# Kernel tuning notes

Measured on AMD Instinct MI355X. Metric: run time of the kernel, lower is better.

## Reference

```python
import jax, jax.numpy as jnp
import numpy as np

H = 256
W = 256
CHUNK = 100  # faces per rasterizer scan step


def _cross2(o, p, q):
    # 2D cross product of (p-o) x (q-o); broadcasts over leading dims
    return (p[..., 0] - o[..., 0]) * (q[..., 1] - o[..., 1]) - (p[..., 1] - o[..., 1]) * (q[..., 0] - o[..., 0])


def transform(verts, K, Rt):
    # verts [B,V,3] -> pixel coords [B,V,3] = (x_pix, y_pix, z_cam)
    v_cam = jnp.einsum('bij,bnj->bni', Rt[:, :, :3], verts) + Rt[:, None, :, 3]
    v_proj = jnp.einsum('bij,bnj->bni', K, v_cam)
    z = v_cam[..., 2:3]
    return jnp.concatenate([v_proj[..., :2] / z, z], axis=-1)


def _pixel_centers(h, w, dtype):
    px = jnp.arange(w, dtype=dtype) + 0.5
    py = jnp.arange(h, dtype=dtype) + 0.5
    gx, gy = jnp.meshgrid(px, py, indexing='xy')  # [h,w]
    return gx, gy


def rasterize(v_pix, vi, h, w):
    # z-buffered triangle rasterization -> index image [B,h,w] (int32, -1 = bg)
    B = v_pix.shape[0]
    Fc = vi.shape[0]
    gx, gy = _pixel_centers(h, w, v_pix.dtype)
    pix = jnp.stack([gx.ravel(), gy.ravel()], axis=-1)  # [HW,2]
    face_ids = jnp.arange(Fc, dtype=jnp.int32).reshape(-1, CHUNK)
    inf = jnp.asarray(jnp.inf, v_pix.dtype)

    def step(carry, fids):
        best_z, best_i = carry
        tri = vi[fids]                      # [C,3]
        p = v_pix[:, tri]                   # [B,C,3,3]
        a, b, c = p[:, :, 0], p[:, :, 1], p[:, :, 2]
        area = _cross2(a[..., :2], b[..., :2], c[..., :2])  # [B,C]
        pixb = pix[None, None]              # [1,1,HW,2]
        w0 = _cross2(b[..., None, :2], c[..., None, :2], pixb)  # [B,C,HW]
        w1 = _cross2(c[..., None, :2], a[..., None, :2], pixb)
        w2 = _cross2(a[..., None, :2], b[..., None, :2], pixb)
        s = jnp.sign(area)[..., None]
        nz = jnp.abs(area)[..., None] > 1e-8
        inside = (w0 * s >= 0) & (w1 * s >= 0) & (w2 * s >= 0) & nz
        za, zb, zc = a[..., 2:3], b[..., 2:3], c[..., 2:3]
        valid = inside & (za > 0) & (zb > 0) & (zc > 0)
        ar = jnp.where(jnp.abs(area) > 1e-8, area, 1.0)[..., None]
        invz = (w0 / ar) / za + (w1 / ar) / zb + (w2 / ar) / zc  # persp-correct 1/z
        z = jnp.where(valid & (invz > 0), 1.0 / jnp.maximum(invz, 1e-12), inf)
        cz = z.min(axis=1)                  # [B,HW]
        ci = z.argmin(axis=1)
        cf = fids[ci]
        upd = cz < best_z
        return (jnp.where(upd, cz, best_z), jnp.where(upd, cf, best_i)), None

    init = (jnp.full((B, h * w), jnp.inf, v_pix.dtype), jnp.full((B, h * w), -1, jnp.int32))
    (_, bi), _ = jax.lax.scan(step, init, face_ids)
    return bi.reshape(B, h, w)


def render(v_pix, vi, index_img):
    # depth [B,h,w] and perspective-correct barycentrics [B,3,h,w]
    B, h, w = index_img.shape
    tri = vi[jnp.clip(index_img, 0)]                 # [B,h,w,3]
    p = jax.vmap(lambda v, t: v[t])(v_pix, tri)      # [B,h,w,3,3]
    gx, gy = _pixel_centers(h, w, v_pix.dtype)
    pt = jnp.stack([gx, gy], axis=-1)[None]          # [1,h,w,2]
    a, b, c = p[..., 0, :], p[..., 1, :], p[..., 2, :]
    w0 = _cross2(b[..., :2], c[..., :2], pt)
    w1 = _cross2(c[..., :2], a[..., :2], pt)
    w2 = _cross2(a[..., :2], b[..., :2], pt)
    area = w0 + w1 + w2
    ar = jnp.where(jnp.abs(area) > 1e-8, area, 1.0)
    f0 = (w0 / ar) / jnp.maximum(a[..., 2], 1e-8)
    f1 = (w1 / ar) / jnp.maximum(b[..., 2], 1e-8)
    f2 = (w2 / ar) / jnp.maximum(c[..., 2], 1e-8)
    invz = f0 + f1 + f2
    invz_s = jnp.where(jnp.abs(invz) > 1e-12, invz, 1.0)
    depth = 1.0 / invz_s
    bary = jnp.stack([f0, f1, f2], axis=-1) / invz_s[..., None]  # [B,h,w,3]
    m = index_img != -1
    depth_img = jnp.where(m, depth, 0.0)
    bary_img = jnp.where(m[..., None], bary, 0.0).transpose(0, 3, 1, 2)  # [B,3,h,w]
    return depth_img, bary_img


def interpolate(attr, vti, index_img, bary_img):
    # attr [B,N,D], bary_img [B,3,h,w] -> [B,D,h,w]
    tri = vti[jnp.clip(index_img, 0)]                # [B,h,w,3]
    av = jax.vmap(lambda a, t: a[t])(attr, tri)      # [B,h,w,3,D]
    return jnp.einsum('bhwkd,bkhw->bdhw', av, bary_img)


def grid_sample_bilinear(tex, grid):
    # tex [B,C,Ht,Wt], grid [B,h,w,2] in [-1,1]; align_corners=False, zero pad
    B, C, Ht, Wt = tex.shape
    x = (grid[..., 0] + 1.0) * Wt / 2.0 - 0.5
    y = (grid[..., 1] + 1.0) * Ht / 2.0 - 0.5
    x0 = jnp.floor(x)
    y0 = jnp.floor(y)
    wx = (x - x0)[:, None]
    wy = (y - y0)[:, None]
    x0i = x0.astype(jnp.int32)
    y0i = y0.astype(jnp.int32)

    def gat(ix, iy):
        valid = (ix >= 0) & (ix < Wt) & (iy >= 0) & (iy < Ht)
        ixc = jnp.clip(ix, 0, Wt - 1)
        iyc = jnp.clip(iy, 0, Ht - 1)
        v = jax.vmap(lambda t, yy, xx: t[:, yy, xx])(tex, iyc, ixc)  # [B,C,h,w]
        return v * valid[:, None].astype(tex.dtype)

    return (gat(x0i, y0i) * (1 - wx) * (1 - wy)
            + gat(x0i + 1, y0i) * wx * (1 - wy)
            + gat(x0i, y0i + 1) * (1 - wx) * wy
            + gat(x0i + 1, y0i + 1) * wx * wy)


def reference(verts, tex, K, Rt, vt, vi, vti):
    v_pix = transform(verts, K, Rt)
    index_img = jax.lax.stop_gradient(rasterize(v_pix, vi, H, W))
    depth_img, bary_img = render(v_pix, vi, index_img)
    B = verts.shape[0]
    vt_attr = jnp.broadcast_to((vt * 2.0 - 1.0)[None], (B,) + vt.shape)
    vt_img = interpolate(vt_attr, vti, index_img, bary_img)    # [B,2,H,W]
    mask = (index_img != -1)[:, None].astype(tex.dtype)
    img = grid_sample_bilinear(tex, vt_img.transpose(0, 2, 3, 1)) * mask
    # edge_grad_estimator is identity in the forward pass
    return img, depth_img, v_pix, vt_img, index_img, bary_img, mask


def setup_inputs() -> dict:
    key = jax.random.key(0)
    ks = jax.random.split(key, 6)
    B, V, Fc, Nvt = 2, 5000, 10000, 5000
    xy = jax.random.uniform(ks[0], (B, V, 2), minval=-1.5, maxval=1.5)
    z = jax.random.uniform(ks[1], (B, V, 1), minval=2.0, maxval=4.0)
    verts = jnp.concatenate([xy, z], axis=-1)
    tex = jax.random.uniform(ks[2], (B, 3, 1024, 1024), dtype=jnp.float32)
    K = jnp.broadcast_to(jnp.array([[256., 0., 128.], [0., 256., 128.], [0., 0., 1.]], dtype=jnp.float32), (B, 3, 3))
    Rt = jnp.broadcast_to(jnp.concatenate([jnp.eye(3, dtype=jnp.float32), jnp.zeros((3, 1), jnp.float32)], axis=1), (B, 3, 4))
    vt = jax.random.uniform(ks[3], (Nvt, 2), dtype=jnp.float32)
    vi = jax.random.randint(ks[4], (Fc, 3), 0, V).astype(jnp.int32)
    vti = jax.random.randint(ks[5], (Fc, 3), 0, Nvt).astype(jnp.int32)
    return {"verts": verts, "tex": tex, "K": K, "Rt": Rt, "vt": vt, "vi": vi, "vti": vti}
```

## Files before the change

kernel.cpp:

```cpp
#include <hip/hip_runtime.h>
#include <cmath>

#define H_ 256
#define W_ 256
#define SEG 4
#define NB 256
#define ILV 8
#define REC_STRIDE 24
#define INITKEY 0x7f800000FFFFFFFFull

__device__ inline unsigned fkey(float f) {
  unsigned u = __float_as_uint(f);
  return (u & 0x80000000u) ? ~u : (u | 0x80000000u);
}
__device__ inline float unfkey(unsigned k) {
  return (k & 0x80000000u) ? __uint_as_float(k & 0x7fffffffu) : __uint_as_float(~k);
}

__global__ void k_transform(const float* __restrict__ verts, const float* __restrict__ Km,
                            const float* __restrict__ Rt, float* __restrict__ vpix,
                            int B, int V) {
  int i = blockIdx.x * blockDim.x + threadIdx.x;
  if (i >= B * V) return;
  int b = i / V;
  float x = verts[(size_t)i * 3 + 0], y = verts[(size_t)i * 3 + 1], z = verts[(size_t)i * 3 + 2];
  const float* R = Rt + (size_t)b * 12;
  float cx = __fadd_rn(__fadd_rn(__fadd_rn(__fmul_rn(R[0], x), __fmul_rn(R[1], y)), __fmul_rn(R[2], z)), R[3]);
  float cy = __fadd_rn(__fadd_rn(__fadd_rn(__fmul_rn(R[4], x), __fmul_rn(R[5], y)), __fmul_rn(R[6], z)), R[7]);
  float cz = __fadd_rn(__fadd_rn(__fadd_rn(__fmul_rn(R[8], x), __fmul_rn(R[9], y)), __fmul_rn(R[10], z)), R[11]);
  const float* Kb = Km + (size_t)b * 9;
  float px = __fadd_rn(__fadd_rn(__fmul_rn(Kb[0], cx), __fmul_rn(Kb[1], cy)), __fmul_rn(Kb[2], cz));
  float py = __fadd_rn(__fadd_rn(__fmul_rn(Kb[3], cx), __fmul_rn(Kb[4], cy)), __fmul_rn(Kb[5], cz));
  vpix[(size_t)i * 3 + 0] = __fdiv_rn(px, cz);
  vpix[(size_t)i * 3 + 1] = __fdiv_rn(py, cz);
  vpix[(size_t)i * 3 + 2] = cz;
}

__global__ void k_init(unsigned long long* __restrict__ keys, int nkeys,
                       int* __restrict__ hist, int* __restrict__ cursor, int nbkt,
                       unsigned* __restrict__ minmax) {
  int i = blockIdx.x * blockDim.x + threadIdx.x;
  if (keys && i < nkeys) keys[i] = INITKEY;
  if (i < nbkt) { hist[i] = 0; cursor[i] = 0; }
  if (i == 0 && minmax) { minmax[0] = 0xFFFFFFFFu; minmax[1] = 0u; }
}

__global__ void k_faceprep(const float* __restrict__ vpix, const int* __restrict__ vi,
                           float* __restrict__ rec, unsigned* __restrict__ minmax,
                           int B, int V, int F) {
  int i = blockIdx.x * blockDim.x + threadIdx.x;
  if (i >= B * F) return;
  int b = i / F, f = i - b * F;
  int i0 = vi[f * 3 + 0], i1 = vi[f * 3 + 1], i2 = vi[f * 3 + 2];
  const float* base = vpix + (size_t)b * V * 3;
  float ax = base[(size_t)i0 * 3], ay = base[(size_t)i0 * 3 + 1], az = base[(size_t)i0 * 3 + 2];
  float bx = base[(size_t)i1 * 3], by = base[(size_t)i1 * 3 + 1], bz = base[(size_t)i1 * 3 + 2];
  float cx = base[(size_t)i2 * 3], cy = base[(size_t)i2 * 3 + 1], cz = base[(size_t)i2 * 3 + 2];
  float e0x = __fsub_rn(cx, bx), e0y = __fsub_rn(cy, by);
  float e1x = __fsub_rn(ax, cx), e1y = __fsub_rn(ay, cy);
  float e2x = __fsub_rn(bx, ax), e2y = __fsub_rn(by, ay);
  float area = __fsub_rn(__fmul_rn(e2x, __fsub_rn(cy, ay)), __fmul_rn(e2y, __fsub_rn(cx, ax)));
  float s = (area > 0.f) ? 1.f : ((area < 0.f) ? -1.f : 0.f);
  bool nz = fabsf(area) > 1e-8f;
  bool zv = (az > 0.f) && (bz > 0.f) && (cz > 0.f);
  float sprime = (nz && zv) ? s : __uint_as_float(0x7fc00000u);
  float ar = nz ? area : 1.0f;
  float zmin = fminf(az, fminf(bz, cz));
  float* r = rec + (size_t)i * REC_STRIDE;
  r[0] = ax; r[1] = ay; r[2] = bx; r[3] = by; r[4] = cx; r[5] = cy;
  r[6] = e0x; r[7] = e0y; r[8] = e1x; r[9] = e1y; r[10] = e2x; r[11] = e2y;
  r[12] = az; r[13] = bz; r[14] = cz; r[15] = sprime; r[16] = ar;
  r[17] = fminf(ax, fminf(bx, cx));
  r[18] = fmaxf(ax, fmaxf(bx, cx));
  r[19] = fminf(ay, fminf(by, cy));
  r[20] = fmaxf(ay, fmaxf(by, cy));
  r[21] = zmin; r[22] = 0.f; r[23] = 0.f;
  if (minmax && zmin == zmin) {
    unsigned k = fkey(zmin);
    atomicMin(&minmax[0], k);
    atomicMax(&minmax[1], k);
  }
}

__global__ void k_hist(const float* __restrict__ rec, const unsigned* __restrict__ minmax,
                       int* __restrict__ hist, int B, int F) {
  int i = blockIdx.x * blockDim.x + threadIdx.x;
  if (i >= B * F) return;
  int b = i / F;
  float zmin = rec[(size_t)i * REC_STRIDE + 21];
  float zlo = unfkey(minmax[0]), zhi = unfkey(minmax[1]);
  float scale = (float)NB / fmaxf(zhi - zlo, 1e-12f);
  int bkt = 0;
  if (zmin == zmin) bkt = min(NB - 1, max(0, (int)((zmin - zlo) * scale)));
  atomicAdd(&hist[b * NB + bkt], 1);
}

__global__ void k_scan(const int* __restrict__ hist, int* __restrict__ boff, int B) {
  __shared__ int sh[NB];
  int t = threadIdx.x;
  for (int b = 0; b < B; ++b) {
    sh[t] = hist[b * NB + t];
    __syncthreads();
    int self = sh[t];
    for (int ofs = 1; ofs < NB; ofs <<= 1) {
      int u = (t >= ofs) ? sh[t - ofs] : 0;
      __syncthreads();
      sh[t] += u;
      __syncthreads();
    }
    boff[b * NB + t] = sh[t] - self;
    __syncthreads();
  }
}

__global__ void k_scatter(const float* __restrict__ rec, const unsigned* __restrict__ minmax,
                          const int* __restrict__ boff, int* __restrict__ cursor,
                          float4* __restrict__ sA, float4* __restrict__ sB4,
                          float4* __restrict__ sC, float4* __restrict__ sZ,
                          float4* __restrict__ sbb, int* __restrict__ sfid,
                          int B, int F) {
  int i = blockIdx.x * blockDim.x + threadIdx.x;
  if (i >= B * F) return;
  int b = i / F, f = i - b * F;
  const float* r = rec + (size_t)i * REC_STRIDE;
  float zmin = r[21];
  float zlo = unfkey(minmax[0]), zhi = unfkey(minmax[1]);
  float rng = fmaxf(zhi - zlo, 1e-12f);
  float scale = (float)NB / rng;
  int bkt = 0;
  if (zmin == zmin) bkt = min(NB - 1, max(0, (int)((zmin - zlo) * scale)));
  int pos = boff[b * NB + bkt] + atomicAdd(&cursor[b * NB + bkt], 1);
  size_t gp = (size_t)b * F + pos;
  float sp = r[15];
  sbb[gp] = make_float4(r[17], r[18], r[19], r[20]);
  sA[gp]  = make_float4(r[0], r[1], r[2], r[3]);
  sB4[gp] = make_float4(r[4], r[5], __fmul_rn(sp, r[6]), __fmul_rn(sp, r[7]));
  sC[gp]  = make_float4(__fmul_rn(sp, r[8]), __fmul_rn(sp, r[9]),
                        __fmul_rn(sp, r[10]), __fmul_rn(sp, r[11]));
  sZ[gp]  = make_float4(r[12], r[13], r[14], __fmul_rn(sp, r[16]));
  sfid[gp] = f;
}

__global__ __launch_bounds__(64 * ILV) void k_raster_tile(const float4* __restrict__ sA,
                                                          const float4* __restrict__ sB4,
                                                          const float4* __restrict__ sC,
                                                          const float4* __restrict__ sZ,
                                                          const float4* __restrict__ sbb,
                                                          const int* __restrict__ sfid,
                                                          const int* __restrict__ boff,
                                                          const unsigned* __restrict__ minmax,
                                                          float* __restrict__ o_idx,
                                                          int B, int F) {
  int seg = blockIdx.x;
  int y   = blockIdx.y;
  int b   = blockIdx.z;
  int tid = threadIdx.x;
  int w = tid >> 6, lane = tid & 63;
  __shared__ unsigned long long sk[64];
  __shared__ int bstart[NB + 1];
  if (tid < 64) sk[tid] = INITKEY;
  if (tid < NB) bstart[tid] = boff[b * NB + tid];
  if (tid == 0) bstart[NB] = F;
  __syncthreads();
  float zlo = unfkey(minmax[0]), zhi = unfkey(minmax[1]);
  float rng = fmaxf(zhi - zlo, 1e-12f);
  float stepv = __fdiv_rn(rng, (float)NB);
  size_t fb = (size_t)b * F;
  float px = seg * 64 + lane + 0.5f, py = y + 0.5f;
  float wx0 = seg * 64 + 0.5f, wx1 = wx0 + 63.0f;
  unsigned long long bestkey = INITKEY;
  int limit = F;
  int it = 0;
  for (int pos = w; pos < limit; pos += ILV) {
    float4 bb = sbb[fb + pos];
    bool cull = (py < bb.z) || (py > bb.w) || (bb.y < wx0) || (bb.x > wx1);
    if (!cull) {
      float4 a0 = sA[fb + pos];
      float4 a1 = sB4[fb + pos];
      float4 a2 = sC[fb + pos];
      float t0 = __fsub_rn(__fmul_rn(a1.z, __fsub_rn(py, a0.w)), __fmul_rn(a1.w, __fsub_rn(px, a0.z)));
      float t1 = __fsub_rn(__fmul_rn(a2.x, __fsub_rn(py, a1.y)), __fmul_rn(a2.y, __fsub_rn(px, a1.x)));
      float t2 = __fsub_rn(__fmul_rn(a2.z, __fsub_rn(py, a0.y)), __fmul_rn(a2.w, __fsub_rn(px, a0.x)));
      bool inside = (t0 >= 0.f) && (t1 >= 0.f) && (t2 >= 0.f);
      if (inside) {
        float4 zz = sZ[fb + pos];
        float u0 = __fdiv_rn(__fdiv_rn(t0, zz.w), zz.x);
        float u1 = __fdiv_rn(__fdiv_rn(t1, zz.w), zz.y);
        float u2 = __fdiv_rn(__fdiv_rn(t2, zz.w), zz.z);
        float invz = __fadd_rn(__fadd_rn(u0, u1), u2);
        if (invz > 0.f) {
          float z = __fdiv_rn(1.0f, fmaxf(invz, 1e-12f));
          int fid = sfid[fb + pos];
          unsigned long long ck = ((unsigned long long)__float_as_uint(z) << 32) | (unsigned)fid;
          if (ck < bestkey) {
            bestkey = ck;
            atomicMin(&sk[lane], ck);
          }
        }
      }
    }
    ++it;
    if ((it & 7) == 0) {
      unsigned long long old = atomicMin(&sk[lane], bestkey);
      if (old < bestkey) bestkey = old;
      float bz = __uint_as_float((unsigned)(bestkey >> 32));
      #pragma unroll
      for (int m = 32; m >= 1; m >>= 1) bz = fmaxf(bz, __shfl_xor(bz, m));
      if (bz < 3.0e38f) {
        float q = __fdiv_rn(__fsub_rn(__fdiv_rn(__fadd_rn(bz, 1e-5f), 0.9999f), zlo), stepv);
        int k = (int)floorf(q) - 2;
        if (k < 0) k = 0;
        while (k < NB &&
               !(__fsub_rn(__fmul_rn(__fadd_rn(zlo, __fmul_rn((float)k, stepv)), 0.9999f), 1e-5f) > bz))
          ++k;
        limit = bstart[k];
      }
    }
  }
  atomicMin(&sk[lane], bestkey);
  __syncthreads();
  if (tid < 64) {
    unsigned long long k = sk[tid];
    unsigned zb = (unsigned)(k >> 32);
    o_idx[(size_t)b * (H_ * W_) + (size_t)y * W_ + seg * 64 + tid] =
        (zb >= 0x7f800000u) ? -1.0f : (float)(int)(unsigned)(k & 0xffffffffu);
  }
}

__global__ __launch_bounds__(256) void k_raster(const float* __restrict__ rec,
                                                unsigned long long* __restrict__ keys,
                                                int B, int F) {
  int x = threadIdx.x;
  int y = blockIdx.x;
  int b = blockIdx.y;
  int seg = blockIdx.z;
  int f0 = (int)((long long)seg * F / SEG);
  int f1 = (int)((long long)(seg + 1) * F / SEG);
  float px = x + 0.5f, py = y + 0.5f;
  float bestz = INFINITY; int besti = -1;
  const float* rb = rec + (size_t)b * F * REC_STRIDE;
  for (int f = f0; f < f1; ++f) {
    const float* r = rb + (size_t)f * REC_STRIDE;
    float miny = r[19], maxy = r[20], minx = r[17], maxx = r[18];
    if (py < miny || py > maxy || maxx < 0.5f || minx > (float)W_ - 0.5f) continue;
    float e0x = r[6], e0y = r[7], e1x = r[8], e1y = r[9], e2x = r[10], e2y = r[11];
    float za = r[12], zb = r[13], zc = r[14], sp = r[15], ar = r[16];
    float w0 = __fsub_rn(__fmul_rn(e0x, __fsub_rn(py, r[3])), __fmul_rn(e0y, __fsub_rn(px, r[2])));
    float w1 = __fsub_rn(__fmul_rn(e1x, __fsub_rn(py, r[5])), __fmul_rn(e1y, __fsub_rn(px, r[4])));
    float w2 = __fsub_rn(__fmul_rn(e2x, __fsub_rn(py, r[1])), __fmul_rn(e2y, __fsub_rn(px, r[0])));
    bool inside = (__fmul_rn(w0, sp) >= 0.f) && (__fmul_rn(w1, sp) >= 0.f) && (__fmul_rn(w2, sp) >= 0.f);
    if (inside) {
      float t0 = __fdiv_rn(__fdiv_rn(w0, ar), za);
      float t1 = __fdiv_rn(__fdiv_rn(w1, ar), zb);
      float t2 = __fdiv_rn(__fdiv_rn(w2, ar), zc);
      float invz = __fadd_rn(__fadd_rn(t0, t1), t2);
      if (invz > 0.f) {
        float z = __fdiv_rn(1.0f, fmaxf(invz, 1e-12f));
        if (z < bestz) { bestz = z; besti = f; }
      }
    }
  }
  if (besti >= 0) {
    unsigned long long key = ((unsigned long long)__float_as_uint(bestz) << 32) | (unsigned)besti;
    atomicMin(&keys[(size_t)b * (H_ * W_) + y * W_ + x], key);
  }
}

__global__ void k_resolve(const unsigned long long* __restrict__ keys, float* __restrict__ idxout, int n) {
  int i = blockIdx.x * blockDim.x + threadIdx.x;
  if (i >= n) return;
  unsigned long long k = keys[i];
  unsigned zb = (unsigned)(k >> 32);
  idxout[i] = (zb >= 0x7f800000u) ? -1.0f : (float)(int)(unsigned)(k & 0xffffffffu);
}

__global__ void k_raster_direct(const float* __restrict__ vpix, const int* __restrict__ vi,
                                float* __restrict__ idxout, int B, int V, int F) {
  int p = blockIdx.x * blockDim.x + threadIdx.x;
  if (p >= B * H_ * W_) return;
  int b = p / (H_ * W_); int pid = p - b * (H_ * W_);
  float px = (pid & (W_ - 1)) + 0.5f, py = (pid >> 8) + 0.5f;
  const float* base = vpix + (size_t)b * V * 3;
  float bestz = INFINITY; int besti = -1;
  for (int f = 0; f < F; ++f) {
    int i0 = vi[f * 3], i1 = vi[f * 3 + 1], i2 = vi[f * 3 + 2];
    float ax = base[(size_t)i0 * 3], ay = base[(size_t)i0 * 3 + 1], za = base[(size_t)i0 * 3 + 2];
    float bx = base[(size_t)i1 * 3], by = base[(size_t)i1 * 3 + 1], zb = base[(size_t)i1 * 3 + 2];
    float cx = base[(size_t)i2 * 3], cy = base[(size_t)i2 * 3 + 1], zc = base[(size_t)i2 * 3 + 2];
    float e0x = __fsub_rn(cx, bx), e0y = __fsub_rn(cy, by);
    float e1x = __fsub_rn(ax, cx), e1y = __fsub_rn(ay, cy);
    float e2x = __fsub_rn(bx, ax), e2y = __fsub_rn(by, ay);
    float area = __fsub_rn(__fmul_rn(e2x, __fsub_rn(cy, ay)), __fmul_rn(e2y, __fsub_rn(cx, ax)));
    float s = (area > 0.f) ? 1.f : ((area < 0.f) ? -1.f : 0.f);
    bool nz = fabsf(area) > 1e-8f;
    bool zv = (za > 0.f) && (zb > 0.f) && (zc > 0.f);
    float sp = (nz && zv) ? s : __uint_as_float(0x7fc00000u);
    float ar = nz ? area : 1.0f;
    float w0 = __fsub_rn(__fmul_rn(e0x, __fsub_rn(py, by)), __fmul_rn(e0y, __fsub_rn(px, bx)));
    float w1 = __fsub_rn(__fmul_rn(e1x, __fsub_rn(py, cy)), __fmul_rn(e1y, __fsub_rn(px, cx)));
    float w2 = __fsub_rn(__fmul_rn(e2x, __fsub_rn(py, ay)), __fmul_rn(e2y, __fsub_rn(px, ax)));
    bool inside = (__fmul_rn(w0, sp) >= 0.f) && (__fmul_rn(w1, sp) >= 0.f) && (__fmul_rn(w2, sp) >= 0.f);
    if (inside) {
      float invz = __fadd_rn(__fadd_rn(__fdiv_rn(__fdiv_rn(w0, ar), za),
                                       __fdiv_rn(__fdiv_rn(w1, ar), zb)),
                             __fdiv_rn(__fdiv_rn(w2, ar), zc));
      if (invz > 0.f) {
        float z = __fdiv_rn(1.0f, fmaxf(invz, 1e-12f));
        if (z < bestz) { bestz = z; besti = f; }
      }
    }
  }
  idxout[p] = (float)besti;
}

__global__ __launch_bounds__(256) void k_render(const float* __restrict__ vpix, const int* __restrict__ vi,
                                                const int* __restrict__ vti, const float* __restrict__ vt,
                                                const float* __restrict__ tex, const float* __restrict__ idxin,
                                                float* __restrict__ o_img, float* __restrict__ o_depth,
                                                float* __restrict__ o_vt, float* __restrict__ o_bary,
                                                float* __restrict__ o_mask,
                                                int B, int V, int F, int TH, int TW) {
  int p = blockIdx.x * blockDim.x + threadIdx.x;
  if (p >= B * H_ * W_) return;
  int HW = H_ * W_;
  int b = p / HW; int pid = p - b * HW;
  int y = pid >> 8, x = pid & (W_ - 1);
  int idx = (int)idxin[p];
  size_t pix2 = (size_t)b * 2 * HW + pid;
  size_t pix3 = (size_t)b * 3 * HW + pid;
  if (idx < 0) {
    o_depth[p] = 0.f; o_mask[p] = 0.f;
    o_vt[pix2] = 0.f; o_vt[pix2 + HW] = 0.f;
    o_bary[pix3] = 0.f; o_bary[pix3 + HW] = 0.f; o_bary[pix3 + 2 * HW] = 0.f;
    o_img[pix3] = 0.f; o_img[pix3 + HW] = 0.f; o_img[pix3 + 2 * HW] = 0.f;
    return;
  }
  const float* base = vpix + (size_t)b * V * 3;
  int i0 = vi[idx * 3], i1 = vi[idx * 3 + 1], i2 = vi[idx * 3 + 2];
  float ax = base[(size_t)i0 * 3], ay = base[(size_t)i0 * 3 + 1], az = base[(size_t)i0 * 3 + 2];
  float bx = base[(size_t)i1 * 3], by = base[(size_t)i1 * 3 + 1], bz = base[(size_t)i1 * 3 + 2];
  float cx = base[(size_t)i2 * 3], cy = base[(size_t)i2 * 3 + 1], cz = base[(size_t)i2 * 3 + 2];
  float ptx = x + 0.5f, pty = y + 0.5f;
  float w0 = __fsub_rn(__fmul_rn(__fsub_rn(cx, bx), __fsub_rn(pty, by)),
                       __fmul_rn(__fsub_rn(cy, by), __fsub_rn(ptx, bx)));
  float w1 = __fsub_rn(__fmul_rn(__fsub_rn(ax, cx), __fsub_rn(pty, cy)),
                       __fmul_rn(__fsub_rn(ay, cy), __fsub_rn(ptx, cx)));
  float w2 = __fsub_rn(__fmul_rn(__fsub_rn(bx, ax), __fsub_rn(pty, ay)),
                       __fmul_rn(__fsub_rn(by, ay), __fsub_rn(ptx, ax)));
  float area = __fadd_rn(__fadd_rn(w0, w1), w2);
  float ar = (fabsf(area) > 1e-8f) ? area : 1.0f;
  float f0 = __fdiv_rn(__fdiv_rn(w0, ar), fmaxf(az, 1e-8f));
  float f1 = __fdiv_rn(__fdiv_rn(w1, ar), fmaxf(bz, 1e-8f));
  float f2 = __fdiv_rn(__fdiv_rn(w2, ar), fmaxf(cz, 1e-8f));
  float invz = __fadd_rn(__fadd_rn(f0, f1), f2);
  float invz_s = (fabsf(invz) > 1e-12f) ? invz : 1.0f;
  float depth = __fdiv_rn(1.0f, invz_s);
  float bary0 = __fdiv_rn(f0, invz_s);
  float bary1 = __fdiv_rn(f1, invz_s);
  float bary2 = __fdiv_rn(f2, invz_s);
  o_depth[p] = depth; o_mask[p] = 1.0f;
  o_bary[pix3] = bary0; o_bary[pix3 + HW] = bary1; o_bary[pix3 + 2 * HW] = bary2;
  int t0 = vti[idx * 3], t1 = vti[idx * 3 + 1], t2 = vti[idx * 3 + 2];
  float u0x = __fsub_rn(__fmul_rn(vt[(size_t)t0 * 2], 2.f), 1.f);
  float u0y = __fsub_rn(__fmul_rn(vt[(size_t)t0 * 2 + 1], 2.f), 1.f);
  float u1x = __fsub_rn(__fmul_rn(vt[(size_t)t1 * 2], 2.f), 1.f);
  float u1y = __fsub_rn(__fmul_rn(vt[(size_t)t1 * 2 + 1], 2.f), 1.f);
  float u2x = __fsub_rn(__fmul_rn(vt[(size_t)t2 * 2], 2.f), 1.f);
  float u2y = __fsub_rn(__fmul_rn(vt[(size_t)t2 * 2 + 1], 2.f), 1.f);
  float gx = __fadd_rn(__fadd_rn(__fmul_rn(u0x, bary0), __fmul_rn(u1x, bary1)), __fmul_rn(u2x, bary2));
  float gy = __fadd_rn(__fadd_rn(__fmul_rn(u0y, bary0), __fmul_rn(u1y, bary1)), __fmul_rn(u2y, bary2));
  o_vt[pix2] = gx; o_vt[pix2 + HW] = gy;
  float sx = __fsub_rn(__fdiv_rn(__fmul_rn(__fadd_rn(gx, 1.0f), (float)TW), 2.0f), 0.5f);
  float sy = __fsub_rn(__fdiv_rn(__fmul_rn(__fadd_rn(gy, 1.0f), (float)TH), 2.0f), 0.5f);
  float x0f = floorf(sx), y0f = floorf(sy);
  float wx = __fsub_rn(sx, x0f), wy = __fsub_rn(sy, y0f);
  float omx = __fsub_rn(1.0f, wx), omy = __fsub_rn(1.0f, wy);
  int x0 = (int)x0f, y0 = (int)y0f;
  int x1 = x0 + 1, y1 = y0 + 1;
  bool v00 = (x0 >= 0) && (x0 < TW) && (y0 >= 0) && (y0 < TH);
  bool v10 = (x1 >= 0) && (x1 < TW) && (y0 >= 0) && (y0 < TH);
  bool v01 = (x0 >= 0) && (x0 < TW) && (y1 >= 0) && (y1 < TH);
  bool v11 = (x1 >= 0) && (x1 < TW) && (y1 >= 0) && (y1 < TH);
  int x0c = min(max(x0, 0), TW - 1), x1c = min(max(x1, 0), TW - 1);
  int y0c = min(max(y0, 0), TH - 1), y1c = min(max(y1, 0), TH - 1);
  const float* tb = tex + (size_t)b * 3 * TH * TW;
  #pragma unroll
  for (int ch = 0; ch < 3; ++ch) {
    const float* tc = tb + (size_t)ch * TH * TW;
    float g00 = v00 ? tc[(size_t)y0c * TW + x0c] : 0.f;
    float g10 = v10 ? tc[(size_t)y0c * TW + x1c] : 0.f;
    float g01 = v01 ? tc[(size_t)y1c * TW + x0c] : 0.f;
    float g11 = v11 ? tc[(size_t)y1c * TW + x1c] : 0.f;
    float r = __fmul_rn(__fmul_rn(g00, omx), omy);
    r = __fadd_rn(r, __fmul_rn(__fmul_rn(g10, wx), omy));
    r = __fadd_rn(r, __fmul_rn(__fmul_rn(g01, omx), wy));
    r = __fadd_rn(r, __fmul_rn(__fmul_rn(g11, wx), wy));
    o_img[pix3 + (size_t)ch * HW] = r;
  }
}

extern "C" void kernel_launch(void* const* d_in, const int* in_sizes, int n_in,
                              void* d_out, int out_size, void* d_ws, size_t ws_size,
                              hipStream_t stream) {
  const float* verts = (const float*)d_in[0];
  const float* tex   = (const float*)d_in[1];
  const float* Km    = (const float*)d_in[2];
  const float* Rt    = (const float*)d_in[3];
  const float* vt    = (const float*)d_in[4];
  const int*   vi    = (const int*)d_in[5];
  const int*   vti   = (const int*)d_in[6];

  int B = in_sizes[2] / 9;
  int V = in_sizes[0] / (3 * B);
  int F = in_sizes[5] / 3;
  long texhw = (long)in_sizes[1] / (B * 3);
  int TH = (int)(sqrt((double)texhw) + 0.5);
  int TW = TH;
  const int HW = H_ * W_;

  float* out = (float*)d_out;
  float* o_img   = out;
  float* o_depth = o_img + (size_t)B * 3 * HW;
  float* o_vpix  = o_depth + (size_t)B * HW;
  float* o_vt    = o_vpix + (size_t)B * V * 3;
  float* o_idx   = o_vt + (size_t)B * 2 * HW;
  float* o_bary  = o_idx + (size_t)B * HW;
  float* o_mask  = o_bary + (size_t)B * 3 * HW;

  k_transform<<<(B * V + 255) / 256, 256, 0, stream>>>(verts, Km, Rt, o_vpix, B, V);

  size_t f4Bytes   = (size_t)B * F * 16;
  size_t recBytes  = (size_t)B * F * REC_STRIDE * 4;
  size_t fidBytes  = (size_t)B * F * 4;
  size_t histBytes = (size_t)B * NB * 4;
  size_t keysBytes = (size_t)B * HW * 8;
  size_t needSorted = 5 * f4Bytes + recBytes + fidBytes + 3 * histBytes + 16;
  size_t needBasic  = keysBytes + recBytes;

  if (ws_size >= needSorted) {
    char* w = (char*)d_ws;
    float4* sA  = (float4*)w;  w += f4Bytes;
    float4* sB4 = (float4*)w;  w += f4Bytes;
    float4* sC  = (float4*)w;  w += f4Bytes;
    float4* sZ  = (float4*)w;  w += f4Bytes;
    float4* sbb = (float4*)w;  w += f4Bytes;
    float*  rec = (float*)w;   w += recBytes;
    int*    sfid = (int*)w;    w += fidBytes;
    int*    hist = (int*)w;    w += histBytes;
    int*    boff = (int*)w;    w += histBytes;
    int*    cursor = (int*)w;  w += histBytes;
    unsigned* minmax = (unsigned*)w;

    k_init<<<(B * NB + 255) / 256, 256, 0, stream>>>((unsigned long long*)nullptr, 0, hist, cursor, B * NB, minmax);
    k_faceprep<<<(B * F + 255) / 256, 256, 0, stream>>>(o_vpix, vi, rec, minmax, B, V, F);
    k_hist<<<(B * F + 255) / 256, 256, 0, stream>>>(rec, minmax, hist, B, F);
    k_scan<<<1, NB, 0, stream>>>(hist, boff, B);
    k_scatter<<<(B * F + 255) / 256, 256, 0, stream>>>(rec, minmax, boff, cursor,
                                                       sA, sB4, sC, sZ, sbb, sfid, B, F);
    dim3 rg(W_ / 64, H_, B);
    k_raster_tile<<<rg, 64 * ILV, 0, stream>>>(sA, sB4, sC, sZ, sbb, sfid, boff, minmax, o_idx, B, F);
  } else if (ws_size >= needBasic) {
    unsigned long long* keys = (unsigned long long*)d_ws;
    float* rec = (float*)((char*)d_ws + keysBytes);
    k_init<<<(B * HW + 255) / 256, 256, 0, stream>>>(keys, B * HW, (int*)nullptr, (int*)nullptr, 0, (unsigned*)nullptr);
    k_faceprep<<<(B * F + 255) / 256, 256, 0, stream>>>(o_vpix, vi, rec, (unsigned*)nullptr, B, V, F);
    dim3 rg(H_, B, SEG);
    k_raster<<<rg, 256, 0, stream>>>(rec, keys, B, F);
    k_resolve<<<(B * HW + 255) / 256, 256, 0, stream>>>(keys, o_idx, B * HW);
  } else {
    k_raster_direct<<<(B * HW + 255) / 256, 256, 0, stream>>>(o_vpix, vi, o_idx, B, V, F);
  }

  k_render<<<(B * HW + 255) / 256, 256, 0, stream>>>(o_vpix, vi, vti, vt, tex, o_idx,
                                                     o_img, o_depth, o_vt, o_bary, o_mask,
                                                     B, V, F, TH, TW);
}
```

Baseline: 454.0 us.

## Replace bucket-limit scan with per-face early exit and prefetch face data

The rasterizer no longer recomputes a bucket limit from a shuffle-reduced max depth and a bucket-start table. Each face record now carries its bucket floor depth, min depth and face id, and each wave breaks out once every lane's best z lies below the current face's floor. Inside faces whose min depth cannot beat the current best skip the perspective divides. The loop also software-prefetches the next face's records, and the interleave drops from 8 to 4 waves per block. This trades one extra float4 load per face and a per-iteration vote for a finer-grained cull and less control overhead.

```diff
diff --git a/kernel.cpp b/kernel.cpp
--- a/kernel.cpp
+++ b/kernel.cpp
@@ -5,7 +5,7 @@
 #define W_ 256
 #define SEG 4
 #define NB 256
-#define ILV 8
+#define ILV 4
 #define REC_STRIDE 24
 #define INITKEY 0x7f800000FFFFFFFFull
 
@@ -116,8 +116,8 @@
 __global__ void k_scatter(const float* __restrict__ rec, const unsigned* __restrict__ minmax,
                           const int* __restrict__ boff, int* __restrict__ cursor,
                           float4* __restrict__ sA, float4* __restrict__ sB4,
-                          float4* __restrict__ sC, float4* __restrict__ sZ,
-                          float4* __restrict__ sbb, int* __restrict__ sfid,
+                          float4* __restrict__ sC, float4* __restrict__ sZ1,
+                          float4* __restrict__ sbb, float4* __restrict__ sM,
                           int B, int F) {
   int i = blockIdx.x * blockDim.x + threadIdx.x;
   if (i >= B * F) return;
@@ -129,26 +129,25 @@
   float scale = (float)NB / rng;
   int bkt = 0;
   if (zmin == zmin) bkt = min(NB - 1, max(0, (int)((zmin - zlo) * scale)));
+  float floorval = zlo + (float)bkt * (rng / (float)NB);
   int pos = boff[b * NB + bkt] + atomicAdd(&cursor[b * NB + bkt], 1);
   size_t gp = (size_t)b * F + pos;
   float sp = r[15];
+  sM[gp]  = make_float4(floorval, zmin, __int_as_float(f), 0.f);
   sbb[gp] = make_float4(r[17], r[18], r[19], r[20]);
   sA[gp]  = make_float4(r[0], r[1], r[2], r[3]);
   sB4[gp] = make_float4(r[4], r[5], __fmul_rn(sp, r[6]), __fmul_rn(sp, r[7]));
   sC[gp]  = make_float4(__fmul_rn(sp, r[8]), __fmul_rn(sp, r[9]),
                         __fmul_rn(sp, r[10]), __fmul_rn(sp, r[11]));
-  sZ[gp]  = make_float4(r[12], r[13], r[14], __fmul_rn(sp, r[16]));
-  sfid[gp] = f;
+  sZ1[gp] = make_float4(r[12], r[13], r[14], __fmul_rn(sp, r[16]));
 }
 
 __global__ __launch_bounds__(64 * ILV) void k_raster_tile(const float4* __restrict__ sA,
                                                           const float4* __restrict__ sB4,
                                                           const float4* __restrict__ sC,
-                                                          const float4* __restrict__ sZ,
+                                                          const float4* __restrict__ sZ1,
                                                           const float4* __restrict__ sbb,
-                                                          const int* __restrict__ sfid,
-                                                          const int* __restrict__ boff,
-                                                          const unsigned* __restrict__ minmax,
+                                                          const float4* __restrict__ sM,
                                                           float* __restrict__ o_idx,
                                                           int B, int F) {
   int seg = blockIdx.x;
@@ -157,65 +156,61 @@
   int tid = threadIdx.x;
   int w = tid >> 6, lane = tid & 63;
   __shared__ unsigned long long sk[64];
-  __shared__ int bstart[NB + 1];
   if (tid < 64) sk[tid] = INITKEY;
-  if (tid < NB) bstart[tid] = boff[b * NB + tid];
-  if (tid == 0) bstart[NB] = F;
   __syncthreads();
-  float zlo = unfkey(minmax[0]), zhi = unfkey(minmax[1]);
-  float rng = fmaxf(zhi - zlo, 1e-12f);
-  float stepv = __fdiv_rn(rng, (float)NB);
   size_t fb = (size_t)b * F;
   float px = seg * 64 + lane + 0.5f, py = y + 0.5f;
   float wx0 = seg * 64 + 0.5f, wx1 = wx0 + 63.0f;
   unsigned long long bestkey = INITKEY;
-  int limit = F;
+  float bestz = INFINITY;
+  int pos = w;
+  float4 M  = sM[fb + pos];
+  float4 bb = sbb[fb + pos];
+  float4 a0 = sA[fb + pos];
+  float4 a1 = sB4[fb + pos];
+  float4 a2 = sC[fb + pos];
   int it = 0;
-  for (int pos = w; pos < limit; pos += ILV) {
-    float4 bb = sbb[fb + pos];
+  while (pos < F) {
+    int nxt = pos + ILV;
+    int nl = (nxt < F) ? nxt : (F - 1);
+    float4 Mn  = sM[fb + nl];
+    float4 bbn = sbb[fb + nl];
+    float4 a0n = sA[fb + nl];
+    float4 a1n = sB4[fb + nl];
+    float4 a2n = sC[fb + nl];
+    float floor0 = __fmul_rn(M.x, 0.9999f) - 1e-5f;
+    if (__all(floor0 > bestz)) break;
+    ++it;
+    if ((it & 7) == 0) {
+      unsigned long long old = atomicMin(&sk[lane], bestkey);
+      if (old < bestkey) { bestkey = old; bestz = __uint_as_float((unsigned)(bestkey >> 32)); }
+    }
     bool cull = (py < bb.z) || (py > bb.w) || (bb.y < wx0) || (bb.x > wx1);
     if (!cull) {
-      float4 a0 = sA[fb + pos];
-      float4 a1 = sB4[fb + pos];
-      float4 a2 = sC[fb + pos];
       float t0 = __fsub_rn(__fmul_rn(a1.z, __fsub_rn(py, a0.w)), __fmul_rn(a1.w, __fsub_rn(px, a0.z)));
       float t1 = __fsub_rn(__fmul_rn(a2.x, __fsub_rn(py, a1.y)), __fmul_rn(a2.y, __fsub_rn(px, a1.x)));
       float t2 = __fsub_rn(__fmul_rn(a2.z, __fsub_rn(py, a0.y)), __fmul_rn(a2.w, __fsub_rn(px, a0.x)));
       bool inside = (t0 >= 0.f) && (t1 >= 0.f) && (t2 >= 0.f);
-      if (inside) {
-        float4 zz = sZ[fb + pos];
+      if (inside && !(__fmul_rn(M.y, 0.9999f) > bestz)) {
+        float4 zz = sZ1[fb + pos];
         float u0 = __fdiv_rn(__fdiv_rn(t0, zz.w), zz.x);
         float u1 = __fdiv_rn(__fdiv_rn(t1, zz.w), zz.y);
         float u2 = __fdiv_rn(__fdiv_rn(t2, zz.w), zz.z);
         float invz = __fadd_rn(__fadd_rn(u0, u1), u2);
         if (invz > 0.f) {
           float z = __fdiv_rn(1.0f, fmaxf(invz, 1e-12f));
-          int fid = sfid[fb + pos];
+          int fid = __float_as_int(M.z);
           unsigned long long ck = ((unsigned long long)__float_as_uint(z) << 32) | (unsigned)fid;
           if (ck < bestkey) {
             bestkey = ck;
+            bestz = z;
             atomicMin(&sk[lane], ck);
           }
         }
       }
     }
-    ++it;
-    if ((it & 7) == 0) {
-      unsigned long long old = atomicMin(&sk[lane], bestkey);
-      if (old < bestkey) bestkey = old;
-      float bz = __uint_as_float((unsigned)(bestkey >> 32));
-      #pragma unroll
-      for (int m = 32; m >= 1; m >>= 1) bz = fmaxf(bz, __shfl_xor(bz, m));
-      if (bz < 3.0e38f) {
-        float q = __fdiv_rn(__fsub_rn(__fdiv_rn(__fadd_rn(bz, 1e-5f), 0.9999f), zlo), stepv);
-        int k = (int)floorf(q) - 2;
-        if (k < 0) k = 0;
-        while (k < NB &&
-               !(__fsub_rn(__fmul_rn(__fadd_rn(zlo, __fmul_rn((float)k, stepv)), 0.9999f), 1e-5f) > bz))
-          ++k;
-        limit = bstart[k];
-      }
-    }
+    pos = nxt;
+    M = Mn; bb = bbn; a0 = a0n; a1 = a1n; a2 = a2n;
   }
   atomicMin(&sk[lane], bestkey);
   __syncthreads();
@@ -431,10 +426,9 @@
 
   size_t f4Bytes   = (size_t)B * F * 16;
   size_t recBytes  = (size_t)B * F * REC_STRIDE * 4;
-  size_t fidBytes  = (size_t)B * F * 4;
   size_t histBytes = (size_t)B * NB * 4;
   size_t keysBytes = (size_t)B * HW * 8;
-  size_t needSorted = 5 * f4Bytes + recBytes + fidBytes + 3 * histBytes + 16;
+  size_t needSorted = 6 * f4Bytes + recBytes + 3 * histBytes + 16;
   size_t needBasic  = keysBytes + recBytes;
 
   if (ws_size >= needSorted) {
@@ -442,10 +436,10 @@
     float4* sA  = (float4*)w;  w += f4Bytes;
     float4* sB4 = (float4*)w;  w += f4Bytes;
     float4* sC  = (float4*)w;  w += f4Bytes;
-    float4* sZ  = (float4*)w;  w += f4Bytes;
+    float4* sZ1 = (float4*)w;  w += f4Bytes;
     float4* sbb = (float4*)w;  w += f4Bytes;
+    float4* sM  = (float4*)w;  w += f4Bytes;
     float*  rec = (float*)w;   w += recBytes;
-    int*    sfid = (int*)w;    w += fidBytes;
     int*    hist = (int*)w;    w += histBytes;
     int*    boff = (int*)w;    w += histBytes;
     int*    cursor = (int*)w;  w += histBytes;
@@ -456,9 +450,9 @@
     k_hist<<<(B * F + 255) / 256, 256, 0, stream>>>(rec, minmax, hist, B, F);
     k_scan<<<1, NB, 0, stream>>>(hist, boff, B);
     k_scatter<<<(B * F + 255) / 256, 256, 0, stream>>>(rec, minmax, boff, cursor,
-                                                       sA, sB4, sC, sZ, sbb, sfid, B, F);
+                                                       sA, sB4, sC, sZ1, sbb, sM, B, F);
     dim3 rg(W_ / 64, H_, B);
-    k_raster_tile<<<rg, 64 * ILV, 0, stream>>>(sA, sB4, sC, sZ, sbb, sfid, boff, minmax, o_idx, B, F);
+    k_raster_tile<<<rg, 64 * ILV, 0, stream>>>(sA, sB4, sC, sZ1, sbb, sM, o_idx, B, F);
   } else if (ws_size >= needBasic) {
     unsigned long long* keys = (unsigned long long*)d_ws;
     float* rec = (float*)((char*)d_ws + keysBytes);
```

Result: slower. 571.6 us (+25.9%).
